# Performance work log

Measured on AMD Instinct MI355X. Metric: run time of the kernel, lower is better.

## Reference

```python
import jax, jax.numpy as jnp
import numpy as np

B, T, C, H = 2, 2048, 1024, 16
D = C // H
EPS = 1e-5

def _layer_norm(x, w, b):
    mu = jnp.mean(x, axis=-1, keepdims=True)
    var = jnp.var(x, axis=-1, keepdims=True)
    return (x - mu) * jax.lax.rsqrt(var + EPS) * w + b

def setup_inputs() -> dict:
    key = jax.random.key(0)
    ks = jax.random.split(key, 8)
    s = 0.02
    return {
        "x": jax.random.normal(ks[0], (B, T, C), jnp.float32),
        "ln1_w": jnp.ones((C,), jnp.float32),
        "ln1_b": jnp.zeros((C,), jnp.float32),
        "wq": jax.random.normal(ks[1], (C, C), jnp.float32) * s,
        "bq": jnp.zeros((C,), jnp.float32),
        "wk": jax.random.normal(ks[2], (C, C), jnp.float32) * s,
        "bk": jnp.zeros((C,), jnp.float32),
        "wv": jax.random.normal(ks[3], (C, C), jnp.float32) * s,
        "bv": jnp.zeros((C,), jnp.float32),
        "wo": jax.random.normal(ks[4], (C, C), jnp.float32) * s,
        "bo": jnp.zeros((C,), jnp.float32),
        "ln2_w": jnp.ones((C,), jnp.float32),
        "ln2_b": jnp.zeros((C,), jnp.float32),
        "w1": jax.random.normal(ks[5], (C, 4 * C), jnp.float32) * s,
        "b1": jnp.zeros((4 * C,), jnp.float32),
        "w2": jax.random.normal(ks[6], (4 * C, C), jnp.float32) * s,
        "b2": jnp.zeros((C,), jnp.float32),
    }

def reference(x, ln1_w, ln1_b, wq, bq, wk, bk, wv, bv, wo, bo,
              ln2_w, ln2_b, w1, b1, w2, b2):
    # --- attention branch ---
    h = _layer_norm(x, ln1_w, ln1_b)
    q = (h @ wq + bq).reshape(B, T, H, D).transpose(0, 2, 1, 3)  # [B,H,T,D]
    k = (h @ wk + bk).reshape(B, T, H, D).transpose(0, 2, 1, 3)
    v = (h @ wv + bv).reshape(B, T, H, D).transpose(0, 2, 1, 3)
    att = jnp.einsum("bhqd,bhkd->bhqk", q, k) * (1.0 / np.sqrt(D))
    causal = jnp.tril(jnp.ones((T, T), dtype=bool))
    att = jnp.where(causal[None, None], att, jnp.float32(-jnp.inf))
    att = jax.nn.softmax(att, axis=-1)
    y = jnp.einsum("bhqk,bhkd->bhqd", att, v)
    y = y.transpose(0, 2, 1, 3).reshape(B, T, C)
    y = y @ wo + bo
    x = x + y
    # --- MLP branch ---
    h = _layer_norm(x, ln2_w, ln2_b)
    h = jax.nn.gelu(h @ w1 + b1, approximate=False)
    h = h @ w2 + b2
    return x + h
```

## Files before the change

### kernel.cpp

```cpp
#include <hip/hip_runtime.h>
#include <hip/hip_bf16.h>
#include <math.h>

#define B_  2
#define T_  2048
#define C_  1024
#define H_  16
#define D_  64
#define BT_ (B_*T_)

typedef __hip_bfloat16 bf16;
typedef short bf16x8 __attribute__((ext_vector_type(8)));
typedef float floatx4 __attribute__((ext_vector_type(4)));

struct alignas(8) bf4 { bf16 v[4]; };

#define GLOAD_LDS16(g, l) __builtin_amdgcn_global_load_lds(            \
    (const __attribute__((address_space(1))) void*)(g),                \
    (__attribute__((address_space(3))) void*)(l), 16, 0, 0)

__global__ __launch_bounds__(256) void ln_bf16_kernel(const float* __restrict__ x,
    const float* __restrict__ w, const float* __restrict__ b,
    bf16* __restrict__ out)
{
    __shared__ float ps[4], ps2[4];
    __shared__ float sm, srs;
    const int row = blockIdx.x;
    const int tid = threadIdx.x;
    float4 v = ((const float4*)(x + (size_t)row * C_))[tid];
    float s  = v.x + v.y + v.z + v.w;
    float s2 = v.x*v.x + v.y*v.y + v.z*v.z + v.w*v.w;
    for (int off = 32; off > 0; off >>= 1) {
        s  += __shfl_down(s,  off);
        s2 += __shfl_down(s2, off);
    }
    const int wid = tid >> 6;
    if ((tid & 63) == 0) { ps[wid] = s; ps2[wid] = s2; }
    __syncthreads();
    if (tid == 0) {
        float ts  = ps[0] + ps[1] + ps[2] + ps[3];
        float ts2 = ps2[0] + ps2[1] + ps2[2] + ps2[3];
        float mean = ts * (1.0f / C_);
        float var  = ts2 * (1.0f / C_) - mean * mean;
        sm  = mean;
        srs = rsqrtf(var + 1e-5f);
    }
    __syncthreads();
    const float mean = sm, rs = srs;
    float4 wv = ((const float4*)w)[tid];
    float4 bv = ((const float4*)b)[tid];
    bf4 o;
    o.v[0] = __float2bfloat16((v.x - mean) * rs * wv.x + bv.x);
    o.v[1] = __float2bfloat16((v.y - mean) * rs * wv.y + bv.y);
    o.v[2] = __float2bfloat16((v.z - mean) * rs * wv.z + bv.z);
    o.v[3] = __float2bfloat16((v.w - mean) * rs * wv.w + bv.w);
    *(bf4*)(out + (size_t)row * C_ + tid * 4) = o;
}

__device__ __forceinline__ void wconv_body(const float* __restrict__ W,
    bf16* __restrict__ Wt, int K, int N, int k0, int n0)
{
    __shared__ float L[64][65];
    const int t = threadIdx.x;
    const int r = t >> 4, c4 = t & 15;
    #pragma unroll
    for (int p = 0; p < 4; ++p) {
        const int kr = p * 16 + r;
        const float4 v = *(const float4*)(W + (size_t)(k0 + kr) * N + n0 + c4 * 4);
        L[kr][c4*4+0] = v.x; L[kr][c4*4+1] = v.y;
        L[kr][c4*4+2] = v.z; L[kr][c4*4+3] = v.w;
    }
    __syncthreads();
    #pragma unroll
    for (int p = 0; p < 4; ++p) {
        const int nr = p * 16 + r;
        bf4 o;
        o.v[0] = __float2bfloat16(L[c4*4+0][nr]);
        o.v[1] = __float2bfloat16(L[c4*4+1][nr]);
        o.v[2] = __float2bfloat16(L[c4*4+2][nr]);
        o.v[3] = __float2bfloat16(L[c4*4+3][nr]);
        *(bf4*)(Wt + (size_t)(n0 + nr) * K + k0 + c4 * 4) = o;
    }
}

__global__ __launch_bounds__(256) void wconv4_kernel(
    const float* __restrict__ wq, const float* __restrict__ wk,
    const float* __restrict__ wv, const float* __restrict__ wo,
    bf16* __restrict__ wqkvT, bf16* __restrict__ woT)
{
    const int z = blockIdx.z;
    const float* W = (z == 0) ? wq : (z == 1) ? wk : (z == 2) ? wv : wo;
    bf16* Wt = (z == 3) ? woT : wqkvT + (size_t)z * 1024 * 1024;
    wconv_body(W, Wt, 1024, 1024, blockIdx.x * 64, blockIdx.y * 64);
}

__global__ __launch_bounds__(256) void wconv2_kernel(
    const float* __restrict__ w1, const float* __restrict__ w2,
    bf16* __restrict__ w1T, bf16* __restrict__ w2T)
{
    if (blockIdx.z == 0)
        wconv_body(w1, w1T, 1024, 4096, blockIdx.x * 64, blockIdx.y * 64);
    else
        wconv_body(w2, w2T, 4096, 1024, blockIdx.y * 64, blockIdx.x * 64);
}

__global__ void bcat_kernel(const float* __restrict__ bq, const float* __restrict__ bk,
                            const float* __restrict__ bv, float* __restrict__ o)
{
    const int i = blockIdx.x * 256 + threadIdx.x;
    float v = (i < 1024) ? bq[i] : (i < 2048 ? bk[i - 1024] : bv[i - 2048]);
    o[i] = v;
}

__global__ __launch_bounds__(256) void splitk_reduce_kernel(
    float* __restrict__ out, const float* __restrict__ p1,
    const float* __restrict__ bias, const float* __restrict__ res)
{
    const size_t i = (size_t)blockIdx.x * 256 + threadIdx.x;
    float4 o = ((const float4*)out)[i];
    const float4 p = ((const float4*)p1)[i];
    const float4 bb = ((const float4*)bias)[i & (C_ / 4 - 1)];
    const float4 xx = ((const float4*)res)[i];
    o.x += p.x + bb.x + xx.x;
    o.y += p.y + bb.y + xx.y;
    o.z += p.z + bb.z + xx.z;
    o.w += p.w + bb.w + xx.w;
    ((float4*)out)[i] = o;
}

template<int TM, int TN, int BK>
__global__ __launch_bounds__(256) void mfma_gemm_t(
    const bf16* __restrict__ A, const bf16* __restrict__ Wt,
    const float* __restrict__ bias, const float* __restrict__ res,
    void* __restrict__ outv, bf16* __restrict__ vT, float* __restrict__ psplit,
    int M, int N, int K, int ldk, int mode)
{
    constexpr int MI = TM / 32;
    constexpr int NJ = TN / 32;
    constexpr int CPR = BK / 8;
    constexpr int NSLOT = (TM + TN) * CPR / 256;
    __shared__ __align__(16) bf16 smem[(TM + TN) * BK];
    bf16* As = smem;
    bf16* Bs = smem + TM * BK;
    const int tid = threadIdx.x;
    const int w = tid >> 6, l = tid & 63;
    const int fm = l & 15, qd = l >> 4;
    const int m0 = blockIdx.x * TM, n0 = blockIdx.y * TN;
    const int bz = blockIdx.z;
    const int wr = (w >> 1) * (TM / 2), wc = (w & 1) * (TN / 2);

    const bf16* Ab = A  + (size_t)bz * K;
    const bf16* Wb = Wt + (size_t)bz * K;

    const bf16* gsrc[NSLOT];
    bf16* ldst[NSLOT];
    #pragma unroll
    for (int p = 0; p < NSLOT; ++p) {
        const int s = tid + p * 256;
        if (s < TM * CPR) {
            const int row = s / CPR, pos = s % CPR;
            const int ch = pos ^ (row & (CPR - 1));
            gsrc[p] = Ab + (size_t)(m0 + row) * ldk + ch * 8;
            ldst[p] = As + s * 8;
        } else {
            const int s2 = s - TM * CPR;
            const int row = s2 / CPR, pos = s2 % CPR;
            const int ch = pos ^ (row & (CPR - 1));
            gsrc[p] = Wb + (size_t)(n0 + row) * ldk + ch * 8;
            ldst[p] = Bs + s2 * 8;
        }
    }

    floatx4 acc[MI][NJ] = {};

    const int nk = K / BK;
    for (int kk = 0; kk < nk; ++kk) {
        const size_t ko = (size_t)kk * BK;
        __syncthreads();
        #pragma unroll
        for (int p = 0; p < NSLOT; ++p)
            GLOAD_LDS16(gsrc[p] + ko, ldst[p]);
        __syncthreads();
        #pragma unroll
        for (int ks = 0; ks < BK / 32; ++ks) {
            bf16x8 af[MI], bfr[NJ];
            #pragma unroll
            for (int i = 0; i < MI; ++i) {
                const int row = wr + i * 16 + fm;
                af[i] = *(const bf16x8*)(As + row * BK
                        + (((ks * 4 + qd) ^ (row & (CPR - 1))) * 8));
            }
            #pragma unroll
            for (int j = 0; j < NJ; ++j) {
                const int row = wc + j * 16 + fm;
                bfr[j] = *(const bf16x8*)(Bs + row * BK
                        + (((ks * 4 + qd) ^ (row & (CPR - 1))) * 8));
            }
            #pragma unroll
            for (int i = 0; i < MI; ++i)
                #pragma unroll
                for (int j = 0; j < NJ; ++j)
                    acc[i][j] = __builtin_amdgcn_mfma_f32_16x16x32_bf16(
                        af[i], bfr[j], acc[i][j], 0, 0, 0);
        }
    }

    const int col0 = n0 + wc;
    const int row0 = m0 + wr;
    const bool isv = (mode == 3) && (col0 >= 2048);
    const bool bounce = (mode == 0) || (mode == 1) || (mode == 3 && !isv);
    __syncthreads();

    if (bounce) {
        constexpr int RM = TM / 2, RN = TN / 2, CHN = RN / 8;
        bf16* eb = smem + w * (RM * RN);
        #pragma unroll
        for (int j = 0; j < NJ; ++j) {
            const int col = col0 + j * 16 + fm;
            const float bb = bias[col];
            const bool isq = (mode == 3) && (col0 + j * 16 < 1024);
            const int lc = j * 16 + fm;
            #pragma unroll
            for (int i = 0; i < MI; ++i) {
                floatx4 a = acc[i][j];
                #pragma unroll
                for (int r = 0; r < 4; ++r) {
                    float vv = a[r] + bb;
                    if (mode == 1) {
                        float zz = vv * (0.7978845608f + 0.0356774081f * vv * vv);
                        zz = fminf(zz, 15.0f);
                        const float e = __expf(2.0f * zz);
                        vv = vv * (e / (e + 1.0f));
                    }
                    if (isq) vv *= 0.125f;
                    const int lr = i * 16 + qd * 4 + r;
                    const int pch = ((lc >> 3) + 2 * qd) & (CHN - 1);
                    eb[lr * RN + pch * 8 + (lc & 7)] = __float2bfloat16(vv);
                }
            }
        }
        bf16* o = (bf16*)outv;
        #pragma unroll
        for (int c = 0; c < RM * RN / 512; ++c) {
            const int idx = c * 64 + l;
            const int row = idx / CHN;
            const int c8  = idx % CHN;
            const int pch = (c8 + 2 * ((row >> 2) & 3)) & (CHN - 1);
            const bf16x8 vv = *(const bf16x8*)(eb + row * RN + pch * 8);
            *(bf16x8*)(o + (size_t)(row0 + row) * N + col0 + c8 * 8) = vv;
        }
    } else {
        #pragma unroll
        for (int j = 0; j < NJ; ++j) {
            const int col = col0 + j * 16 + fm;
            const float bb = bias[col];
            #pragma unroll
            for (int i = 0; i < MI; ++i) {
                const int row = row0 + i * 16 + qd * 4;
                floatx4 a = acc[i][j];
                if (mode == 4) {
                    float* o = bz ? psplit : (float*)outv;
                    #pragma unroll
                    for (int r = 0; r < 4; ++r)
                        o[(size_t)(row + r) * N + col] = a[r];
                } else if (mode == 2) {
                    float* o = (float*)outv;
                    #pragma unroll
                    for (int r = 0; r < 4; ++r)
                        o[(size_t)(row + r) * N + col] =
                            a[r] + bb + res[(size_t)(row + r) * N + col];
                } else {
                    bf4 pv;
                    #pragma unroll
                    for (int r = 0; r < 4; ++r) pv.v[r] = __float2bfloat16(a[r] + bb);
                    *(bf4*)(vT + (size_t)(col - 2048) * M + row) = pv;
                }
            }
        }
    }
}


#define G8_BARRIER() do {                                   \
    asm volatile("" ::: "memory");                          \
    __builtin_amdgcn_s_barrier();                           \
    asm volatile("" ::: "memory");                          \
  } while (0)

#define G8_WAIT_VM(n) asm volatile("s_waitcnt vmcnt(" #n ")" ::: "memory")

#define G8_VW2() do { if (st1) G8_WAIT_VM(8); else G8_WAIT_VM(2); } while (0)
#define G8_VW3() do { if (st1) G8_WAIT_VM(8); else G8_WAIT_VM(0); } while (0)
#define G8_VW1() do { if (st2) G8_WAIT_VM(8); else if (st1) G8_WAIT_VM(4); \
                      else G8_WAIT_VM(0); } while (0)

#define G8_PHASE(CB, Aq, Bq, RA, RB, SC, SG, DB, KO, VW)                       \
  do {                                                                         \
    if (RA) {                                                                  \
      const bf16* pa0 = smem + (CB) * BUF + aof0 + (Aq) * 8192;                \
      const bf16* pa1 = smem + (CB) * BUF + aof1 + (Aq) * 8192;                \
      _Pragma("unroll")                                                        \
      for (int i = 0; i < 4; ++i) {                                            \
        ar[Aq][i][0] = *(const bf16x8*)(pa0 + i * 1024);                       \
        ar[Aq][i][1] = *(const bf16x8*)(pa1 + i * 1024);                       \
      }                                                                        \
    }                                                                          \
    if (RB) {                                                                  \
      const bf16* pb0 = smem + (CB) * BUF + bof0 + (Bq) * 2048;                \
      const bf16* pb1 = smem + (CB) * BUF + bof1 + (Bq) * 2048;                \
      _Pragma("unroll")                                                        \
      for (int jj = 0; jj < 2; ++jj) {                                         \
        br[jj][0] = *(const bf16x8*)(pb0 + jj * 1024);                         \
        br[jj][1] = *(const bf16x8*)(pb1 + jj * 1024);                         \
      }                                                                        \
    }                                                                          \
    if (SC) {                                                                  \
      GLOAD_LDS16(gsrc[SG] + (KO), smem + (DB) * BUF + lof[SG]);               \
      GLOAD_LDS16(gsrc[SG] + (KO) + (((SG) & 1) ? gdB : gdA),                  \
                  smem + (DB) * BUF + lof[SG] + (((SG) & 1) ? 8192 : 4096));   \
    }                                                                          \
    G8_BARRIER();                                                              \
    __builtin_amdgcn_s_setprio(1);                                             \
    _Pragma("unroll")                                                          \
    for (int i = 0; i < 4; ++i)                                                \
      _Pragma("unroll")                                                        \
      for (int jj = 0; jj < 2; ++jj) {                                         \
        acc[(Aq)*4+i][(Bq)*2+jj] = __builtin_amdgcn_mfma_f32_16x16x32_bf16(    \
            ar[Aq][i][0], br[jj][0], acc[(Aq)*4+i][(Bq)*2+jj], 0, 0, 0);       \
        acc[(Aq)*4+i][(Bq)*2+jj] = __builtin_amdgcn_mfma_f32_16x16x32_bf16(    \
            ar[Aq][i][1], br[jj][1], acc[(Aq)*4+i][(Bq)*2+jj], 0, 0, 0);       \
      }                                                                        \
    __builtin_amdgcn_s_setprio(0);                                             \
    VW;                                                                        \
    G8_BARRIER();                                                              \
  } while (0)

#define G8_TILE(CB, TT)                                                        \
  do {                                                                         \
    const bool st1 = (TT) + 1 < nt;                                            \
    const bool st2 = (TT) + 2 < nt;                                            \
    const size_t ko1 = (size_t)((TT) + 1) * 64;                                \
    const size_t ko2 = (size_t)((TT) + 2) * 64;                                \
    G8_PHASE(CB, 0, 0, 1, 1, st1, 2, (CB) ^ 1, ko1, G8_VW2());                 \
    G8_PHASE(CB, 1, 0, 1, 0, st1, 3, (CB) ^ 1, ko1, G8_VW3());                 \
    G8_PHASE(CB, 0, 1, 0, 1, st2, 1, (CB),     ko2, ;);                        \
    G8_PHASE(CB, 1, 1, 0, 0, st2, 0, (CB),     ko2, G8_VW1());                 \
  } while (0)

template<int MODE>
__global__ __launch_bounds__(512, 2) void gemm8_t(
    const bf16* __restrict__ A, const bf16* __restrict__ Wt,
    const float* __restrict__ bias, bf16* __restrict__ out,
    bf16* __restrict__ vT, int M, int N, int K)
{
    constexpr int BUF = 32768;
    __shared__ __align__(16) bf16 smem[2 * BUF];

    const int tid = threadIdx.x;
    const int w = tid >> 6, l = tid & 63;
    const int fm = l & 15, qd = l >> 4;
    const int wm = w >> 2, wn = w & 3;

    const int nbx = gridDim.x;
    const int nwg = nbx * gridDim.y;
    const int bid = blockIdx.y * nbx + blockIdx.x;
    const int cpx = nwg >> 3;
    const int swz = (bid & 7) * cpx + (bid >> 3);
    const int m0 = (swz % nbx) * 256;
    const int n0 = (swz / nbx) * 256;

    const size_t gdA = (size_t)64 * K;
    const size_t gdB = (size_t)128 * K;
    const bf16* gsrc[4];
    int lof[4];
    #pragma unroll
    for (int g = 0; g < 4; ++g) {
        const int isB  = (g & 1);
        const int half = (g >> 1);
        const int pos = tid & 7;
        int row, lofe;
        const bf16* gb;
        if (!isB) {
            row  = half * 128 + (tid >> 3);
            gb   = A + (size_t)(m0 + row) * K;
            lofe = row * 64 + pos * 8;
        } else {
            const int vr = tid >> 3;
            row  = (vr >> 5) * 64 + half * 32 + (vr & 31);
            gb   = Wt + (size_t)(n0 + row) * K;
            lofe = 16384 + row * 64 + pos * 8;
        }
        const int ch = pos ^ (row & 7);
        gsrc[g] = gb + ch * 8;
        lof[g]  = lofe;
    }

    const int sw0 = qd ^ (fm & 7);
    const int aof0 = (wm * 64 + fm) * 64 + sw0 * 8;
    const int aof1 = (wm * 64 + fm) * 64 + (sw0 ^ 4) * 8;
    const int bof0 = 16384 + (wn * 64 + fm) * 64 + sw0 * 8;
    const int bof1 = 16384 + (wn * 64 + fm) * 64 + (sw0 ^ 4) * 8;

    floatx4 acc[8][4] = {};
    bf16x8 ar[2][4][2];
    bf16x8 br[2][2];

    GLOAD_LDS16(gsrc[0],       smem + lof[0]);
    GLOAD_LDS16(gsrc[0] + gdA, smem + lof[0] + 4096);
    GLOAD_LDS16(gsrc[1],       smem + lof[1]);
    GLOAD_LDS16(gsrc[1] + gdB, smem + lof[1] + 8192);
    GLOAD_LDS16(gsrc[2],       smem + lof[2]);
    GLOAD_LDS16(gsrc[2] + gdA, smem + lof[2] + 4096);
    GLOAD_LDS16(gsrc[3],       smem + lof[3]);
    GLOAD_LDS16(gsrc[3] + gdB, smem + lof[3] + 8192);
    GLOAD_LDS16(gsrc[1] + 64,       smem + BUF + lof[1]);
    GLOAD_LDS16(gsrc[1] + 64 + gdB, smem + BUF + lof[1] + 8192);
    GLOAD_LDS16(gsrc[0] + 64,       smem + BUF + lof[0]);
    GLOAD_LDS16(gsrc[0] + 64 + gdA, smem + BUF + lof[0] + 4096);
    G8_WAIT_VM(8);
    G8_BARRIER();

    const int nt = K / 64;
    for (int t = 0; t < nt; t += 2) {
        G8_TILE(0, t);
        G8_TILE(1, t + 1);
    }

    G8_WAIT_VM(0);
    G8_BARRIER();

    const int colb = n0 + wn * 64;
    if (MODE == 3 && colb >= 2048) {
        #pragma unroll
        for (int jf = 0; jf < 4; ++jf) {
            const int col = colb + jf * 16 + fm;
            const float bb = bias[col];
            #pragma unroll
            for (int f = 0; f < 8; ++f) {
                const int row = m0 + (f >> 2) * 128 + wm * 64 + (f & 3) * 16 + qd * 4;
                bf4 pv;
                #pragma unroll
                for (int r = 0; r < 4; ++r)
                    pv.v[r] = __float2bfloat16(acc[f][jf][r] + bb);
                *(bf4*)(vT + (size_t)(col - 2048) * M + row) = pv;
            }
        }
    } else {
        const float scale = (MODE == 3 && colb < 1024) ? 0.125f : 1.0f;
        bf16* eb = smem + w * 8192;
        #pragma unroll
        for (int jf = 0; jf < 4; ++jf) {
            const int col = colb + jf * 16 + fm;
            const float bb = bias[col];
            const int lc = jf * 16 + fm;
            const int pch = ((lc >> 3) + 2 * qd) & 7;
            #pragma unroll
            for (int f = 0; f < 8; ++f) {
                const int lr = (f & 3) * 16 + qd * 4;
                #pragma unroll
                for (int r = 0; r < 4; ++r) {
                    float vv = acc[f][jf][r] + bb;
                    if (MODE == 1) {
                        float zz = vv * (0.7978845608f + 0.0356774081f * vv * vv);
                        zz = fminf(zz, 15.0f);
                        const float e = __expf(2.0f * zz);
                        vv = vv * (e / (e + 1.0f));
                    }
                    vv *= scale;
                    eb[(f >> 2) * 4096 + (lr + r) * 64 + pch * 8 + (lc & 7)] =
                        __float2bfloat16(vv);
                }
            }
        }
        #pragma unroll
        for (int p = 0; p < 2; ++p)
            #pragma unroll
            for (int c = 0; c < 8; ++c) {
                const int idx = c * 64 + l;
                const int row = idx >> 3, c8 = idx & 7;
                const int pch = (c8 + 2 * ((row >> 2) & 3)) & 7;
                const bf16x8 vv = *(const bf16x8*)(eb + p * 4096 + row * 64 + pch * 8);
                const int rowg = m0 + p * 128 + wm * 64 + row;
                *(bf16x8*)(out + (size_t)rowg * N + colb + c8 * 8) = vv;
            }
    }
}

__global__ __launch_bounds__(256) void attn_mfma_kernel(
    const bf16* __restrict__ qkv, const bf16* __restrict__ vT,
    bf16* __restrict__ y)
{
    const int pi = blockIdx.x, h = blockIdx.y, b = blockIdx.z;
    const int tid = threadIdx.x, w = tid >> 6, l = tid & 63;
    const int fm = l & 15, qd = l >> 4;
    const int qta = pi, qtb = 31 - pi;
    const float M0 = 3.0f;

    __shared__ __align__(16) bf16 Ks[4096];
    __shared__ __align__(16) bf16 Vs[4096];
    __shared__ __align__(16) bf16 Ps[8][1152];

    const int r0 = tid >> 2,         c0 = (tid & 3) ^ ((r0 >> 1) & 3);
    const int r1 = (tid + 256) >> 2, c1 = ((tid + 256) & 3) ^ ((r1 >> 1) & 3);
    const bf16* kbase = qkv + (size_t)(b * T_) * 3072 + 1024 + h * 64;
    const bf16* vbase = vT + (size_t)(h * 64) * BT_ + b * T_;
    const bf16* kg0 = kbase + (size_t)(r0 & 63) * 3072 + (r0 >> 6) * 32 + c0 * 8;
    const bf16* kg1 = kbase + (size_t)(r1 & 63) * 3072 + (r1 >> 6) * 32 + c1 * 8;
    const bf16* vg0 = vbase + (size_t)(r0 & 63) * BT_ + (r0 >> 6) * 32 + c0 * 8;
    const bf16* vg1 = vbase + (size_t)(r1 & 63) * BT_ + (r1 >> 6) * 32 + c1 * 8;
    bf16* ksl0 = Ks + (size_t)(w * 64) * 8;
    bf16* ksl1 = Ks + (size_t)(w * 64 + 256) * 8;
    bf16* vsl0 = Vs + (size_t)(w * 64) * 8;
    bf16* vsl1 = Vs + (size_t)(w * 64 + 256) * 8;

    const bf16* qpa = qkv + (size_t)(b * T_ + qta * 64 + w * 16 + fm) * 3072 + h * 64 + qd * 8;
    const bf16* qpb = qkv + (size_t)(b * T_ + qtb * 64 + w * 16 + fm) * 3072 + h * 64 + qd * 8;
    const bf16x8 qa0 = *(const bf16x8*)qpa, qa1 = *(const bf16x8*)(qpa + 32);
    const bf16x8 qb0 = *(const bf16x8*)qpb, qb1 = *(const bf16x8*)(qpb + 32);

    const int qba = qta * 64 + w * 16 + qd * 4;
    const int qbb = qtb * 64 + w * 16 + qd * 4;
    const int sw = (qd ^ ((fm >> 1) & 3)) * 8;

    float la[4] = {}, lb[4] = {};
    floatx4 Oa[4] = {}, Ob[4] = {};
    bf16* psa = &Ps[w * 2][0];
    bf16* psb = &Ps[w * 2 + 1][0];

    auto tile = [&](const bf16x8 q0, const bf16x8 q1, float* lsum,
                    floatx4* O, bf16* ps, const int kt, const int qt, const int qb) {
        floatx4 S[4];
        #pragma unroll
        for (int nt = 0; nt < 4; ++nt) {
            const int rr = nt * 16 + fm;
            const bf16x8 k0 = *(const bf16x8*)(Ks + rr * 32 + sw);
            const bf16x8 k1 = *(const bf16x8*)(Ks + (64 + rr) * 32 + sw);
            floatx4 s = {};
            s = __builtin_amdgcn_mfma_f32_16x16x32_bf16(q0, k0, s, 0, 0, 0);
            s = __builtin_amdgcn_mfma_f32_16x16x32_bf16(q1, k1, s, 0, 0, 0);
            S[nt] = s;
        }
        if (kt == qt) {
            #pragma unroll
            for (int nt = 0; nt < 4; ++nt) {
                const int key = kt * 64 + nt * 16 + fm;
                #pragma unroll
                for (int r = 0; r < 4; ++r)
                    if (key > qb + r) S[nt][r] = -1e30f;
            }
        }
        #pragma unroll
        for (int nt = 0; nt < 4; ++nt)
            #pragma unroll
            for (int r = 0; r < 4; ++r) {
                const float p = __expf(S[nt][r] - M0);
                lsum[r] += p;
                ps[(qd * 4 + r) * 72 + nt * 16 + fm] = __float2bfloat16(p);
            }
        #pragma unroll
        for (int s2 = 0; s2 < 2; ++s2) {
            const bf16x8 pf = *(const bf16x8*)(ps + fm * 72 + s2 * 32 + qd * 8);
            #pragma unroll
            for (int nt = 0; nt < 4; ++nt) {
                const bf16x8 vf =
                    *(const bf16x8*)(Vs + (s2 * 64 + nt * 16 + fm) * 32 + sw);
                O[nt] = __builtin_amdgcn_mfma_f32_16x16x32_bf16(pf, vf, O[nt], 0, 0, 0);
            }
        }
    };

    for (int kt = 0; kt <= qtb; ++kt) {
        const size_t kOff = (size_t)kt * 64 * 3072;
        const size_t vOff = (size_t)kt * 64;
        __syncthreads();
        GLOAD_LDS16(kg0 + kOff, ksl0);
        GLOAD_LDS16(kg1 + kOff, ksl1);
        GLOAD_LDS16(vg0 + vOff, vsl0);
        GLOAD_LDS16(vg1 + vOff, vsl1);
        __syncthreads();
        tile(qb0, qb1, lb, Ob, psb, kt, qtb, qbb);
        if (kt <= qta)
            tile(qa0, qa1, la, Oa, psa, kt, qta, qba);
    }

    #pragma unroll
    for (int mk = 1; mk < 16; mk <<= 1)
        #pragma unroll
        for (int r = 0; r < 4; ++r) {
            la[r] += __shfl_xor(la[r], mk);
            lb[r] += __shfl_xor(lb[r], mk);
        }

    #pragma unroll
    for (int r = 0; r < 4; ++r) {
        const float inva = 1.0f / la[r];
        const float invb = 1.0f / lb[r];
        const size_t rowa = (size_t)(b * T_) + qba + r;
        const size_t rowb = (size_t)(b * T_) + qbb + r;
        #pragma unroll
        for (int nt = 0; nt < 4; ++nt) {
            y[rowa * C_ + h * 64 + nt * 16 + fm] = __float2bfloat16(Oa[nt][r] * inva);
            y[rowb * C_ + h * 64 + nt * 16 + fm] = __float2bfloat16(Ob[nt][r] * invb);
        }
    }
}

extern "C" void kernel_launch(void* const* d_in, const int* in_sizes, int n_in,
                              void* d_out, int out_size, void* d_ws, size_t ws_size,
                              hipStream_t stream)
{
    const float* x     = (const float*)d_in[0];
    const float* ln1_w = (const float*)d_in[1];
    const float* ln1_b = (const float*)d_in[2];
    const float* wq    = (const float*)d_in[3];
    const float* bq    = (const float*)d_in[4];
    const float* wk    = (const float*)d_in[5];
    const float* bk    = (const float*)d_in[6];
    const float* wv    = (const float*)d_in[7];
    const float* bv    = (const float*)d_in[8];
    const float* wo    = (const float*)d_in[9];
    const float* bo    = (const float*)d_in[10];
    const float* ln2_w = (const float*)d_in[11];
    const float* ln2_b = (const float*)d_in[12];
    const float* w1    = (const float*)d_in[13];
    const float* b1    = (const float*)d_in[14];
    const float* w2    = (const float*)d_in[15];
    const float* b2    = (const float*)d_in[16];
    float* out = (float*)d_out;

    char* ws = (char*)d_ws;
    const size_t MB = 1024 * 1024;
    bf16*  wqkvT = (bf16*)(ws);
    bf16*  woT   = (bf16*)(ws + 6 * MB);
    bf16*  w1T   = (bf16*)(ws + 8 * MB);
    bf16*  w2T   = (bf16*)(ws + 16 * MB);
    float* bqkv  = (float*)(ws + 24 * MB);
    bf16*  h     = (bf16*)(ws + 24 * MB + 65536);
    bf16*  qkv   = (bf16*)(ws + 32 * MB + 65536);
    bf16*  vT    = (bf16*)(ws + 56 * MB + 65536);
    bf16*  y     = (bf16*)(ws + 64 * MB + 65536);
    float* x2    = (float*)(ws + 72 * MB + 65536);
    bf16*  u     = qkv;
    float* p1    = (float*)ws;

    wconv4_kernel<<<dim3(16, 16, 4), 256, 0, stream>>>(wq, wk, wv, wo, wqkvT, woT);
    wconv2_kernel<<<dim3(16, 64, 2), 256, 0, stream>>>(w1, w2, w1T, w2T);
    bcat_kernel<<<12, 256, 0, stream>>>(bq, bk, bv, bqkv);

    ln_bf16_kernel<<<BT_, 256, 0, stream>>>(x, ln1_w, ln1_b, h);
    gemm8_t<3><<<dim3(16, 12), 512, 0, stream>>>(
        h, wqkvT, bqkv, qkv, vT, BT_, 3072, C_);
    attn_mfma_kernel<<<dim3(16, H_, B_), 256, 0, stream>>>(qkv, vT, y);
    mfma_gemm_t<128, 64, 64><<<dim3(32, 16), 256, 0, stream>>>(
        y, woT, bo, x, x2, nullptr, nullptr, BT_, C_, C_, C_, 2);

    ln_bf16_kernel<<<BT_, 256, 0, stream>>>(x2, ln2_w, ln2_b, h);
    gemm8_t<1><<<dim3(16, 16), 512, 0, stream>>>(
        h, w1T, b1, u, nullptr, BT_, 4 * C_, C_);
    mfma_gemm_t<128, 128, 64><<<dim3(32, 8, 2), 256, 0, stream>>>(
        u, w2T, b2, nullptr, out, nullptr, p1, BT_, C_, 2 * C_, 4 * C_, 4);
    splitk_reduce_kernel<<<BT_ * C_ / 1024, 256, 0, stream>>>(out, p1, b2, x2);
}
```

Measured before the change: 350.6 us.

## Merge prep kernels into one launch and replace split-K reduce with atomics

Weight conversion, bias concat, the first layernorm and zeroing of the output are merged into a single prep kernel that branches on block index, cutting several launches. The split-K second MLP GEMM now atomically adds both halves into the zeroed output, with bias and residual added by the first split. This removes the separate reduce kernel and the partial-sum buffer round trip. In exchange it adds atomic traffic, a zeroing pass, and a summation order that is no longer fixed.

New measurement: 361.1 us. 1.03x slower.

```diff
diff --git a/kernel.cpp b/kernel.cpp
--- a/kernel.cpp
+++ b/kernel.cpp
@@ -19,13 +19,12 @@
     (const __attribute__((address_space(1))) void*)(g),                \
     (__attribute__((address_space(3))) void*)(l), 16, 0, 0)
 
-__global__ __launch_bounds__(256) void ln_bf16_kernel(const float* __restrict__ x,
+__device__ __forceinline__ void ln_body(const float* __restrict__ x,
     const float* __restrict__ w, const float* __restrict__ b,
-    bf16* __restrict__ out)
+    bf16* __restrict__ out, const int row)
 {
     __shared__ float ps[4], ps2[4];
     __shared__ float sm, srs;
-    const int row = blockIdx.x;
     const int tid = threadIdx.x;
     float4 v = ((const float4*)(x + (size_t)row * C_))[tid];
     float s  = v.x + v.y + v.z + v.w;
@@ -57,6 +56,13 @@
     *(bf4*)(out + (size_t)row * C_ + tid * 4) = o;
 }
 
+__global__ __launch_bounds__(256) void ln_bf16_kernel(const float* __restrict__ x,
+    const float* __restrict__ w, const float* __restrict__ b,
+    bf16* __restrict__ out)
+{
+    ln_body(x, w, b, out, blockIdx.x);
+}
+
 __device__ __forceinline__ void wconv_body(const float* __restrict__ W,
     bf16* __restrict__ Wt, int K, int N, int k0, int n0)
 {
@@ -83,49 +89,38 @@
     }
 }
 
-__global__ __launch_bounds__(256) void wconv4_kernel(
+__global__ __launch_bounds__(256) void prep_kernel(
+    const float* __restrict__ x, const float* __restrict__ ln1_w,
+    const float* __restrict__ ln1_b,
     const float* __restrict__ wq, const float* __restrict__ wk,
     const float* __restrict__ wv, const float* __restrict__ wo,
-    bf16* __restrict__ wqkvT, bf16* __restrict__ woT)
-{
-    const int z = blockIdx.z;
-    const float* W = (z == 0) ? wq : (z == 1) ? wk : (z == 2) ? wv : wo;
-    bf16* Wt = (z == 3) ? woT : wqkvT + (size_t)z * 1024 * 1024;
-    wconv_body(W, Wt, 1024, 1024, blockIdx.x * 64, blockIdx.y * 64);
-}
-
-__global__ __launch_bounds__(256) void wconv2_kernel(
+    const float* __restrict__ bq, const float* __restrict__ bk,
+    const float* __restrict__ bv,
     const float* __restrict__ w1, const float* __restrict__ w2,
-    bf16* __restrict__ w1T, bf16* __restrict__ w2T)
-{
-    if (blockIdx.z == 0)
-        wconv_body(w1, w1T, 1024, 4096, blockIdx.x * 64, blockIdx.y * 64);
-    else
-        wconv_body(w2, w2T, 4096, 1024, blockIdx.y * 64, blockIdx.x * 64);
-}
-
-__global__ void bcat_kernel(const float* __restrict__ bq, const float* __restrict__ bk,
-                            const float* __restrict__ bv, float* __restrict__ o)
-{
-    const int i = blockIdx.x * 256 + threadIdx.x;
-    float v = (i < 1024) ? bq[i] : (i < 2048 ? bk[i - 1024] : bv[i - 2048]);
-    o[i] = v;
-}
-
-__global__ __launch_bounds__(256) void splitk_reduce_kernel(
-    float* __restrict__ out, const float* __restrict__ p1,
-    const float* __restrict__ bias, const float* __restrict__ res)
-{
-    const size_t i = (size_t)blockIdx.x * 256 + threadIdx.x;
-    float4 o = ((const float4*)out)[i];
-    const float4 p = ((const float4*)p1)[i];
-    const float4 bb = ((const float4*)bias)[i & (C_ / 4 - 1)];
-    const float4 xx = ((const float4*)res)[i];
-    o.x += p.x + bb.x + xx.x;
-    o.y += p.y + bb.y + xx.y;
-    o.z += p.z + bb.z + xx.z;
-    o.w += p.w + bb.w + xx.w;
-    ((float4*)out)[i] = o;
+    bf16* __restrict__ h, bf16* __restrict__ wqkvT, bf16* __restrict__ woT,
+    bf16* __restrict__ w1T, bf16* __restrict__ w2T,
+    float* __restrict__ bqkv, float* __restrict__ outz)
+{
+    const int b = blockIdx.x;
+    if (b < 1024) {
+        const int z = b >> 8, rem = b & 255;
+        const float* W = (z == 0) ? wq : (z == 1) ? wk : (z == 2) ? wv : wo;
+        bf16* Wt = (z == 3) ? woT : wqkvT + (size_t)z * 1024 * 1024;
+        wconv_body(W, Wt, 1024, 1024, (rem & 15) * 64, (rem >> 4) * 64);
+    } else if (b < 3072) {
+        const int c = b - 1024, z = c >> 10, r = c & 1023;
+        if (z == 0) wconv_body(w1, w1T, 1024, 4096, (r & 15) * 64, (r >> 4) * 64);
+        else        wconv_body(w2, w2T, 4096, 1024, (r >> 4) * 64, (r & 15) * 64);
+    } else if (b < 7168) {
+        ln_body(x, ln1_w, ln1_b, h, b - 3072);
+    } else if (b < 7180) {
+        const int i = (b - 7168) * 256 + threadIdx.x;
+        float v = (i < 1024) ? bq[i] : (i < 2048 ? bk[i - 1024] : bv[i - 2048]);
+        bqkv[i] = v;
+    } else {
+        const size_t i = (size_t)(b - 7180) * 256 + threadIdx.x;
+        ((float4*)outz)[i] = make_float4(0.f, 0.f, 0.f, 0.f);
+    }
 }
 
 template<int TM, int TN, int BK>
@@ -258,7 +253,15 @@
             for (int i = 0; i < MI; ++i) {
                 const int row = row0 + i * 16 + qd * 4;
                 floatx4 a = acc[i][j];
-                if (mode == 4) {
+                if (mode == 5) {
+                    float* o = (float*)outv;
+                    #pragma unroll
+                    for (int r = 0; r < 4; ++r) {
+                        float v = a[r];
+                        if (bz == 0) v += bb + res[(size_t)(row + r) * N + col];
+                        atomicAdd(&o[(size_t)(row + r) * N + col], v);
+                    }
+                } else if (mode == 4) {
                     float* o = bz ? psplit : (float*)outv;
                     #pragma unroll
                     for (int r = 0; r < 4; ++r)
@@ -641,13 +644,11 @@
     bf16*  y     = (bf16*)(ws + 64 * MB + 65536);
     float* x2    = (float*)(ws + 72 * MB + 65536);
     bf16*  u     = qkv;
-    float* p1    = (float*)ws;
-
-    wconv4_kernel<<<dim3(16, 16, 4), 256, 0, stream>>>(wq, wk, wv, wo, wqkvT, woT);
-    wconv2_kernel<<<dim3(16, 64, 2), 256, 0, stream>>>(w1, w2, w1T, w2T);
-    bcat_kernel<<<12, 256, 0, stream>>>(bq, bk, bv, bqkv);
-
-    ln_bf16_kernel<<<BT_, 256, 0, stream>>>(x, ln1_w, ln1_b, h);
+
+    prep_kernel<<<11276, 256, 0, stream>>>(
+        x, ln1_w, ln1_b, wq, wk, wv, wo, bq, bk, bv, w1, w2,
+        h, wqkvT, woT, w1T, w2T, bqkv, out);
+
     gemm8_t<3><<<dim3(16, 12), 512, 0, stream>>>(
         h, wqkvT, bqkv, qkv, vT, BT_, 3072, C_);
     attn_mfma_kernel<<<dim3(16, H_, B_), 256, 0, stream>>>(qkv, vT, y);
@@ -658,6 +659,5 @@
     gemm8_t<1><<<dim3(16, 16), 512, 0, stream>>>(
         h, w1T, b1, u, nullptr, BT_, 4 * C_, C_);
     mfma_gemm_t<128, 128, 64><<<dim3(32, 8, 2), 256, 0, stream>>>(
-        u, w2T, b2, nullptr, out, nullptr, p1, BT_, C_, 2 * C_, 4 * C_, 4);
-    splitk_reduce_kernel<<<BT_ * C_ / 1024, 256, 0, stream>>>(out, p1, b2, x2);
-}
+        u, w2T, b2, x2, out, nullptr, nullptr, BT_, C_, 2 * C_, 4 * C_, 5);
+}
```
